# Kernel optimization log

Hardware: AMD Instinct MI355X
Metric: run time of the kernel (lower is better)

The kernel has to match this reference:

```python
import jax, jax.numpy as jnp
import numpy as np

D = 256; NH = 8; NL = 4; NP = 4; DFF = 1024
SHAPES = [(100, 100), (50, 50), (25, 25), (13, 13)]
B = 4


def layer_norm(x, g, b, eps=1e-5):
    m = x.mean(-1, keepdims=True)
    v = ((x - m) ** 2).mean(-1, keepdims=True)
    return (x - m) * jax.lax.rsqrt(v + eps) * g + b


def setup_inputs() -> dict:
    key = jax.random.key(0)
    ks = jax.random.split(key, 12)
    Lin = sum(h * w for h, w in SHAPES)  # 13294
    w = lambda k, s: jax.random.normal(k, s, jnp.float32) * 0.02
    return dict(
        src=jax.random.normal(ks[0], (B, Lin, D), jnp.float32),
        pos=0.1 * jax.random.normal(ks[1], (B, Lin, D), jnp.float32),
        reference_points=jax.random.uniform(ks[2], (B, Lin, NL, 2), dtype=jnp.float32),
        spatial_shapes=jnp.array(SHAPES, jnp.int32),
        level_start_index=jnp.array(np.cumsum([0] + [h * w for h, w in SHAPES])[:-1], jnp.int32),
        value_w=w(ks[3], (D, D)), value_b=jnp.zeros((D,), jnp.float32),
        offs_w=w(ks[4], (D, NH * NL * NP * 2)),
        offs_b=0.5 * jax.random.normal(ks[5], (NH * NL * NP * 2,), jnp.float32),
        attn_w=w(ks[6], (D, NH * NL * NP)), attn_b=jnp.zeros((NH * NL * NP,), jnp.float32),
        out_w=w(ks[7], (D, D)), out_b=jnp.zeros((D,), jnp.float32),
        ln1_g=jnp.ones((D,), jnp.float32), ln1_b=jnp.zeros((D,), jnp.float32),
        ff1_w=w(ks[8], (D, DFF)), ff1_b=jnp.zeros((DFF,), jnp.float32),
        ff2_w=w(ks[9], (DFF, D)), ff2_b=jnp.zeros((D,), jnp.float32),
        ln2_g=jnp.ones((D,), jnp.float32), ln2_b=jnp.zeros((D,), jnp.float32),
    )


def msda(query, value_in, ref, shapes, starts, value_w, value_b, offs_w, offs_b,
         attn_w, attn_b, out_w, out_b):
    Bq, Lq, Dm = query.shape
    dh = Dm // NH
    shapes_np = np.asarray(shapes); starts_np = np.asarray(starts)
    value = (value_in @ value_w + value_b).reshape(Bq, -1, NH, dh)
    offs = (query @ offs_w + offs_b).reshape(Bq, Lq, NH, NL, NP, 2)
    aw = jax.nn.softmax((query @ attn_w + attn_b).reshape(Bq, Lq, NH, NL * NP), axis=-1)
    aw = aw.reshape(Bq, Lq, NH, NL, NP)
    # offset normalizer is (W, H) per level
    normalizer = jnp.stack([shapes[:, 1], shapes[:, 0]], -1).astype(jnp.float32)
    loc = ref[:, :, None, :, None, :] + offs / normalizer[None, None, None, :, None, :]
    out = jnp.zeros((Bq, NH, Lq, dh), jnp.float32)
    for l in range(NL):
        Hl, Wl = int(shapes_np[l, 0]), int(shapes_np[l, 1])
        s = int(starts_np[l])
        v = value[:, s:s + Hl * Wl].transpose(0, 2, 1, 3)  # [B,h,HW,dh]
        x = loc[:, :, :, l, :, 0] * Wl - 0.5  # [B,Lq,h,P], align_corners=False
        y = loc[:, :, :, l, :, 1] * Hl - 0.5
        x0 = jnp.floor(x); y0 = jnp.floor(y)
        dx = x - x0; dy = y - y0
        x0i = x0.astype(jnp.int32); y0i = y0.astype(jnp.int32)
        def gather(ix, iy):
            valid = (ix >= 0) & (ix < Wl) & (iy >= 0) & (iy < Hl)  # zero padding
            idx = jnp.clip(iy, 0, Hl - 1) * Wl + jnp.clip(ix, 0, Wl - 1)
            idx = idx.transpose(0, 2, 1, 3).reshape(Bq, NH, Lq * NP)
            g = jnp.take_along_axis(v, idx[..., None], axis=2).reshape(Bq, NH, Lq, NP, dh)
            return g * valid.transpose(0, 2, 1, 3)[..., None]
        dxh = dx.transpose(0, 2, 1, 3)[..., None]
        dyh = dy.transpose(0, 2, 1, 3)[..., None]
        sampled = (gather(x0i, y0i) * (1 - dxh) * (1 - dyh)
                   + gather(x0i + 1, y0i) * dxh * (1 - dyh)
                   + gather(x0i, y0i + 1) * (1 - dxh) * dyh
                   + gather(x0i + 1, y0i + 1) * dxh * dyh)  # [B,h,Lq,P,dh]
        awl = aw[:, :, :, l].transpose(0, 2, 1, 3)[..., None]  # [B,h,Lq,P,1]
        out = out + (sampled * awl).sum(3)
    out = out.transpose(0, 2, 1, 3).reshape(Bq, Lq, Dm)
    return out @ out_w + out_b


def reference(src, pos, reference_points, spatial_shapes, level_start_index,
              value_w, value_b, offs_w, offs_b, attn_w, attn_b, out_w, out_b,
              ln1_g, ln1_b, ff1_w, ff1_b, ff2_w, ff2_b, ln2_g, ln2_b):
    # src = with_pos_embed(src, pos): NOTE this module uses (src + pos) as BOTH query and value
    q = src + pos
    src2 = msda(q, q, reference_points, spatial_shapes, level_start_index,
                value_w, value_b, offs_w, offs_b, attn_w, attn_b, out_w, out_b)
    x = layer_norm(q + src2, ln1_g, ln1_b)  # dropout is identity at eval
    ff = jnp.maximum(x @ ff1_w + ff1_b, 0.0) @ ff2_w + ff2_b
    return layer_norm(x + ff, ln2_g, ln2_b)
```

## Files before the change

### kernel.cpp

```cpp
#include <hip/hip_runtime.h>
#include <hip/hip_bf16.h>

#define B_    4
#define LIN   13294
#define M_    (B_*LIN)
#define D_    256
#define NH_   8
#define NL_   4
#define NP_   4
#define DFF_  1024

typedef __bf16 bf16;
typedef unsigned int uint;
typedef __attribute__((ext_vector_type(8))) __bf16 bfrag8;
typedef __attribute__((ext_vector_type(4))) __bf16 bf16x4;
typedef __attribute__((ext_vector_type(4))) float facc4;
typedef __attribute__((ext_vector_type(2))) float f32x2;

__global__ __launch_bounds__(256) void make_q(const float* __restrict__ src,
                                              const float* __restrict__ pos,
                                              float* __restrict__ q,
                                              bf16* __restrict__ qb, int n4) {
  int i = blockIdx.x * 256 + threadIdx.x;
  if (i >= n4) return;
  float4 s = ((const float4*)src)[i];
  float4 p = ((const float4*)pos)[i];
  float4 v = {s.x + p.x, s.y + p.y, s.z + p.z, s.w + p.w};
  ((float4*)q)[i] = v;
  bf16 t4[4] = {(bf16)v.x, (bf16)v.y, (bf16)v.z, (bf16)v.w};
  ((uint2*)qb)[i] = *(uint2*)t4;
}

__global__ __launch_bounds__(256) void prep_weights(
    const float* __restrict__ vw, const float* __restrict__ ow,
    const float* __restrict__ aw, const float* __restrict__ outw,
    const float* __restrict__ f1w, const float* __restrict__ f2w,
    const float* __restrict__ vb, const float* __restrict__ ob,
    const float* __restrict__ ab,
    bf16* __restrict__ vowt, bf16* __restrict__ outwt,
    bf16* __restrict__ f1wt, bf16* __restrict__ f2wt, float* __restrict__ vobias) {
  int seg = blockIdx.y;
  int idx = blockIdx.x * 256 + threadIdx.x;
  if (seg == 6) {
    if (idx < 256) vobias[idx] = vb[idx];
    else if (idx < 512) vobias[idx] = ob[idx - 256];
    else if (idx < 640) vobias[idx] = ab[idx - 512];
    return;
  }
  const float* W; bf16* Wt; int K, N;
  switch (seg) {
    case 0: W = vw;   Wt = vowt;              K = 256;  N = 256;  break;
    case 1: W = ow;   Wt = vowt + 256 * 256;  K = 256;  N = 256;  break;
    case 2: W = aw;   Wt = vowt + 512 * 256;  K = 256;  N = 128;  break;
    case 3: W = outw; Wt = outwt;             K = 256;  N = 256;  break;
    case 4: W = f1w;  Wt = f1wt;              K = 256;  N = 1024; break;
    default: W = f2w; Wt = f2wt;              K = 1024; N = 256;  break;
  }
  if (idx < K * N) {
    int n = idx / K, k = idx - n * K;
    Wt[idx] = (bf16)W[k * N + n];
  }
}

__device__ __forceinline__ void gload16(const bf16* g, bf16* l) {
  __builtin_amdgcn_global_load_lds(
      (const __attribute__((address_space(1))) uint*)g,
      (__attribute__((address_space(3))) uint*)l, 16, 0, 0);
}

template<int K, bool RELU>
__global__ __launch_bounds__(256) void gemm128(
    const bf16* __restrict__ A, const bf16* __restrict__ Bt,
    const float* __restrict__ bias, bf16* __restrict__ C,
    int Mdim, int N) {
  __shared__ __align__(16) bf16 As[128 * 64];
  __shared__ __align__(16) bf16 Bs[128 * 64];
  const int t = threadIdx.x, wave = t >> 6, lane = t & 63;
  const int m0 = blockIdx.x * 128, n0 = blockIdx.y * 128;
  const int wr = wave >> 1, wc = wave & 1;
  const int ln = lane & 15, quad = lane >> 4;
  const int sr = lane >> 3, cc = lane & 7;
  const int gcol = (cc ^ sr) * 8;

  const bf16* ap[4]; const bf16* bp[4];
  bf16* la[4]; bf16* lb[4];
  #pragma unroll
  for (int ii = 0; ii < 4; ii++) {
    int i = wave * 4 + ii;
    int arow = min(m0 + i * 8 + sr, Mdim - 1);
    ap[ii] = A + (size_t)arow * K + gcol;
    bp[ii] = Bt + (size_t)(n0 + i * 8 + sr) * K + gcol;
    la[ii] = As + i * 512;
    lb[ii] = Bs + i * 512;
  }
  int a_off[4], b_off[4];
  #pragma unroll
  for (int i = 0; i < 4; i++) {
    int ra = wr * 64 + i * 16 + ln;
    int rb = wc * 64 + i * 16 + ln;
    a_off[i] = ra * 128 + ((quad ^ (ra & 7)) * 16);
    b_off[i] = rb * 128 + ((quad ^ (rb & 7)) * 16);
  }

  facc4 acc[4][4];
  #pragma unroll
  for (int mt = 0; mt < 4; mt++)
    #pragma unroll
    for (int nt = 0; nt < 4; nt++) acc[mt][nt] = (facc4){0.f, 0.f, 0.f, 0.f};

  #pragma unroll 1
  for (int k0 = 0; k0 < K; k0 += 64) {
    __syncthreads();
    gload16(ap[0] + k0, la[0]); gload16(ap[1] + k0, la[1]);
    gload16(ap[2] + k0, la[2]); gload16(ap[3] + k0, la[3]);
    gload16(bp[0] + k0, lb[0]); gload16(bp[1] + k0, lb[1]);
    gload16(bp[2] + k0, lb[2]); gload16(bp[3] + k0, lb[3]);
    __syncthreads();
    #pragma unroll
    for (int ks = 0; ks < 2; ks++) {
      bfrag8 wfr[4], xfr[4];
      #pragma unroll
      for (int nt = 0; nt < 4; nt++)
        wfr[nt] = *(const bfrag8*)((const char*)Bs + (b_off[nt] ^ (ks * 64)));
      #pragma unroll
      for (int mt = 0; mt < 4; mt++)
        xfr[mt] = *(const bfrag8*)((const char*)As + (a_off[mt] ^ (ks * 64)));
      #pragma unroll
      for (int mt = 0; mt < 4; mt++)
        #pragma unroll
        for (int nt = 0; nt < 4; nt++)
          acc[mt][nt] = __builtin_amdgcn_mfma_f32_16x16x32_bf16(wfr[nt], xfr[mt], acc[mt][nt], 0, 0, 0);
    }
  }

  #pragma unroll
  for (int nt = 0; nt < 4; nt++) {
    int ncol = n0 + wc * 64 + nt * 16 + quad * 4;
    float4 bv = *(const float4*)&bias[ncol];
    #pragma unroll
    for (int mt = 0; mt < 4; mt++) {
      int row = m0 + wr * 64 + mt * 16 + ln;
      if (row < Mdim) {
        float v0 = acc[mt][nt][0] + bv.x, v1 = acc[mt][nt][1] + bv.y;
        float v2 = acc[mt][nt][2] + bv.z, v3 = acc[mt][nt][3] + bv.w;
        if (RELU) {
          v0 = fmaxf(v0, 0.f); v1 = fmaxf(v1, 0.f);
          v2 = fmaxf(v2, 0.f); v3 = fmaxf(v3, 0.f);
        }
        bf16 o[4] = {(bf16)v0, (bf16)v1, (bf16)v2, (bf16)v3};
        *(uint2*)&C[(size_t)row * N + ncol] = *(uint2*)o;
      }
    }
  }
}

__global__ __launch_bounds__(256) void msda_sample(
    const bf16* __restrict__ VOA,
    const float* __restrict__ ref,
    bf16* __restrict__ sampled) {
  int gw = (blockIdx.x * 256 + threadIdx.x) >> 6;
  int lane = threadIdx.x & 63;
  int m = gw >> 3, h = gw & 7;
  if (m >= M_) return;
  int b = m / LIN;
  int p = lane >> 2, cg = lane & 3;
  int l = p >> 2, pt = p & 3;
  int Wl = (l == 0) ? 100 : (l == 1) ? 50 : (l == 2) ? 25 : 13;
  int Hl = Wl;
  int st = (l == 0) ? 0 : (l == 1) ? 10000 : (l == 2) ? 12500 : 13125;

  const bf16* row = VOA + (size_t)m * 640;
  float e = __expf((float)row[512 + h * 16 + p]);
  float se = e;
  #pragma unroll
  for (int msk = 4; msk < 64; msk <<= 1) se += __shfl_xor(se, msk);
  float w = e / se;

  float rx = ref[((size_t)m * 4 + l) * 2 + 0];
  float ry = ref[((size_t)m * 4 + l) * 2 + 1];
  uint oxy = *(const uint*)&row[256 + ((h * 4 + l) * 4 + pt) * 2];
  float ox = __uint_as_float(oxy << 16);
  float oy = __uint_as_float(oxy & 0xffff0000u);
  float x = rx * (float)Wl + ox - 0.5f;
  float y = ry * (float)Hl + oy - 0.5f;
  float x0f = floorf(x), y0f = floorf(y);
  float dx = x - x0f, dy = y - y0f;
  int x0 = (int)x0f, y0 = (int)y0f;
  float wx1 = 1.f - dx, wy1 = 1.f - dy;

  f32x2 acc2[4];
  #pragma unroll
  for (int i = 0; i < 4; i++) acc2[i] = (f32x2){0.f, 0.f};

  size_t vbase = ((size_t)(b * LIN + st)) * 640 + h * 32 + cg * 8;
  #pragma unroll
  for (int c = 0; c < 4; c++) {
    int cx = c & 1, cy = c >> 1;
    int xi = x0 + cx, yi = y0 + cy;
    bool valid = (xi >= 0) & (xi < Wl) & (yi >= 0) & (yi < Hl);
    int xc = min(max(xi, 0), Wl - 1);
    int yc = min(max(yi, 0), Hl - 1);
    float cw = (cx ? dx : wx1) * (cy ? dy : wy1) * w;
    cw = valid ? cw : 0.f;
    uint off = (uint)(yc * Wl + xc) * 640u;
    const uint4 vv = *(const uint4*)(VOA + vbase + off);
    f32x2 cw2 = {cw, cw};
    f32x2 v0 = {__uint_as_float(vv.x << 16), __uint_as_float(vv.x & 0xffff0000u)};
    f32x2 v1 = {__uint_as_float(vv.y << 16), __uint_as_float(vv.y & 0xffff0000u)};
    f32x2 v2 = {__uint_as_float(vv.z << 16), __uint_as_float(vv.z & 0xffff0000u)};
    f32x2 v3 = {__uint_as_float(vv.w << 16), __uint_as_float(vv.w & 0xffff0000u)};
    acc2[0] = cw2 * v0 + acc2[0];
    acc2[1] = cw2 * v1 + acc2[1];
    acc2[2] = cw2 * v2 + acc2[2];
    acc2[3] = cw2 * v3 + acc2[3];
  }

  int sel = (lane >> 2) & 1;
  f32x2 sA0 = sel ? acc2[0] : acc2[2];
  f32x2 sA1 = sel ? acc2[1] : acc2[3];
  f32x2 kA0 = sel ? acc2[2] : acc2[0];
  f32x2 kA1 = sel ? acc2[3] : acc2[1];
  f32x2 rA0, rA1;
  rA0.x = __shfl_xor(sA0.x, 4); rA0.y = __shfl_xor(sA0.y, 4);
  rA1.x = __shfl_xor(sA1.x, 4); rA1.y = __shfl_xor(sA1.y, 4);
  kA0 += rA0; kA1 += rA1;

  int sel2 = (lane >> 3) & 1;
  f32x2 sB = sel2 ? kA0 : kA1;
  f32x2 kB = sel2 ? kA1 : kA0;
  f32x2 rB;
  rB.x = __shfl_xor(sB.x, 8); rB.y = __shfl_xor(sB.y, 8);
  kB += rB;

  int sel3 = (lane >> 4) & 1;
  float sC = sel3 ? kB.x : kB.y;
  float kC = sel3 ? kB.y : kB.x;
  kC += __shfl_xor(sC, 16);

  float v = kC + __shfl_xor(kC, 32);

  if (lane < 32) {
    int c = cg * 8 + ((lane >> 2) & 1) * 4 + ((lane >> 3) & 1) * 2 + ((lane >> 4) & 1);
    sampled[(size_t)m * 256 + h * 32 + c] = (bf16)v;
  }
}

__device__ inline float4 load4f(const float* p) { return *(const float4*)p; }
__device__ inline float4 load4f(const bf16* p) {
  bf16x4 v = *(const bf16x4*)p;
  float4 r = {(float)v[0], (float)v[1], (float)v[2], (float)v[3]};
  return r;
}
template<typename RT>
__global__ __launch_bounds__(256) void ln_kernel(
    const bf16* __restrict__ a, const RT* __restrict__ res,
    const float* __restrict__ g, const float* __restrict__ beta,
    float* __restrict__ out_f, bf16* __restrict__ out_b, int Mdim) {
  int wave = threadIdx.x >> 6, lane = threadIdx.x & 63;
  int row = blockIdx.x * 4 + wave;
  if (row >= Mdim) return;
  size_t base = (size_t)row * 256 + lane * 4;
  float4 av = load4f(a + base);
  float4 rv = load4f(res + base);
  float4 v = {av.x + rv.x, av.y + rv.y, av.z + rv.z, av.w + rv.w};
  float s = v.x + v.y + v.z + v.w;
  #pragma unroll
  for (int msk = 1; msk < 64; msk <<= 1) s += __shfl_xor(s, msk);
  float mean = s * (1.f / 256.f);
  float4 d = {v.x - mean, v.y - mean, v.z - mean, v.w - mean};
  float sq = d.x * d.x + d.y * d.y + d.z * d.z + d.w * d.w;
  #pragma unroll
  for (int msk = 1; msk < 64; msk <<= 1) sq += __shfl_xor(sq, msk);
  float inv = rsqrtf(sq * (1.f / 256.f) + 1e-5f);
  float4 gv = *(const float4*)(g + lane * 4);
  float4 bv = *(const float4*)(beta + lane * 4);
  float4 y = {d.x * inv * gv.x + bv.x, d.y * inv * gv.y + bv.y,
              d.z * inv * gv.z + bv.z, d.w * inv * gv.w + bv.w};
  if (out_f) *(float4*)(out_f + base) = y;
  if (out_b) {
    bf16 t4[4] = {(bf16)y.x, (bf16)y.y, (bf16)y.z, (bf16)y.w};
    *(uint2*)(out_b + base) = *(uint2*)t4;
  }
}

extern "C" void kernel_launch(void* const* d_in, const int* in_sizes, int n_in,
                              void* d_out, int out_size, void* d_ws, size_t ws_size,
                              hipStream_t stream) {
  const float* src     = (const float*)d_in[0];
  const float* pos     = (const float*)d_in[1];
  const float* refpts  = (const float*)d_in[2];
  const float* value_w = (const float*)d_in[5];
  const float* value_b = (const float*)d_in[6];
  const float* offs_w  = (const float*)d_in[7];
  const float* offs_b  = (const float*)d_in[8];
  const float* attn_w  = (const float*)d_in[9];
  const float* attn_b  = (const float*)d_in[10];
  const float* out_w   = (const float*)d_in[11];
  const float* out_b   = (const float*)d_in[12];
  const float* ln1_g   = (const float*)d_in[13];
  const float* ln1_b   = (const float*)d_in[14];
  const float* ff1_w   = (const float*)d_in[15];
  const float* ff1_b   = (const float*)d_in[16];
  const float* ff2_w   = (const float*)d_in[17];
  const float* ff2_b   = (const float*)d_in[18];
  const float* ln2_g   = (const float*)d_in[19];
  const float* ln2_b   = (const float*)d_in[20];

  char* ws = (char*)d_ws;
  size_t off = 0;
  auto take = [&](size_t bytes) -> char* {
    char* pp = ws + off;
    off += (bytes + 255) & ~(size_t)255;
    return pp;
  };
  float* q      = (float*)take((size_t)M_ * 256 * 4);
  size_t szQB   = (size_t)M_ * 256 * 2;
  size_t szVOA  = (size_t)M_ * 640 * 2;
  char* R       = take(szQB + szVOA + szQB);
  bf16* qb      = (bf16*)R;
  bf16* VOA     = (bf16*)(R + szQB);
  bf16* sampled = (bf16*)(R + szQB + szVOA);
  bf16* hb      = (bf16*)R;
  bf16* tmp     = (bf16*)take(szQB);
  bf16* x       = (bf16*)take(szQB);
  bf16* vowt    = (bf16*)take(640 * 256 * 2);
  bf16* outwt   = (bf16*)take(65536 * 2);
  bf16* f1wt    = (bf16*)take(262144 * 2);
  bf16* f2wt    = (bf16*)take(262144 * 2);
  float* vobias = (float*)take(640 * 4);
  (void)ws_size; (void)in_sizes; (void)n_in; (void)out_size;

  int n4 = M_ * 256 / 4;
  make_q<<<dim3((n4 + 255) / 256), dim3(256), 0, stream>>>(src, pos, q, qb, n4);
  prep_weights<<<dim3(1024, 7), dim3(256), 0, stream>>>(
      value_w, offs_w, attn_w, out_w, ff1_w, ff2_w, value_b, offs_b, attn_b,
      vowt, outwt, f1wt, f2wt, vobias);

  dim3 blk(256);
  int mt = (M_ + 127) / 128;
  gemm128<256, false><<<dim3(mt, 5), blk, 0, stream>>>(qb, vowt, vobias, VOA, M_, 640);
  msda_sample<<<dim3(M_ * 2), blk, 0, stream>>>(VOA, refpts, sampled);
  gemm128<256, false><<<dim3(mt, 2), blk, 0, stream>>>(sampled, outwt, out_b, tmp, M_, 256);
  ln_kernel<float><<<dim3((M_ + 3) / 4), blk, 0, stream>>>(tmp, q, ln1_g, ln1_b, nullptr, x, M_);
  gemm128<256, true><<<dim3(mt, 8), blk, 0, stream>>>(x, f1wt, ff1_b, hb, M_, 1024);
  gemm128<1024, false><<<dim3(mt, 2), blk, 0, stream>>>(hb, f2wt, ff2_b, tmp, M_, 256);
  ln_kernel<bf16><<<dim3((M_ + 3) / 4), blk, 0, stream>>>(tmp, x, ln2_g, ln2_b, (float*)d_out, nullptr, M_);
}
```

Measured before the change: 582.3 us.

## Restructure GEMMs to stage full-K A tile once and stream weights from global

Replaces the 128x128 LDS-tiled GEMM with a kernel where each block stages a 128xK(256-chunk) slice of A into padded LDS once and loops over all N columns. Weight fragments are read directly from global/L2 rather than through LDS, and grid drops the N dimension so A is read only once per row block. The change cuts redundant A traffic and per-k-step barriers, but it increases global weight loads per block, lowers parallelism (one block per 128 rows), and for K=1024 holds NB*8 accumulators in registers. The sampler also hoists its four corner loads ahead of the FMAs to expose more memory-level parallelism.

```diff
diff --git a/kernel.cpp b/kernel.cpp
--- a/kernel.cpp
+++ b/kernel.cpp
@@ -62,95 +62,115 @@
   }
 }
 
-__device__ __forceinline__ void gload16(const bf16* g, bf16* l) {
-  __builtin_amdgcn_global_load_lds(
-      (const __attribute__((address_space(1))) uint*)g,
-      (__attribute__((address_space(3))) uint*)l, 16, 0, 0);
-}
-
-template<int K, bool RELU>
-__global__ __launch_bounds__(256) void gemm128(
-    const bf16* __restrict__ A, const bf16* __restrict__ Bt,
-    const float* __restrict__ bias, bf16* __restrict__ C,
-    int Mdim, int N) {
-  __shared__ __align__(16) bf16 As[128 * 64];
-  __shared__ __align__(16) bf16 Bs[128 * 64];
+template<int K, int N, bool RELU>
+__global__ __launch_bounds__(256) void gemm_fused(
+    const bf16* __restrict__ A, const bf16* __restrict__ Wt,
+    const float* __restrict__ bias, bf16* __restrict__ C, int Mdim) {
+  static_assert(K % 256 == 0 && N % 64 == 0, "shape");
+  constexpr int NB = N / 64;
+  constexpr int PITCH = 264;
+  __shared__ __align__(16) bf16 As[128 * PITCH];
   const int t = threadIdx.x, wave = t >> 6, lane = t & 63;
-  const int m0 = blockIdx.x * 128, n0 = blockIdx.y * 128;
-  const int wr = wave >> 1, wc = wave & 1;
+  const int m0 = blockIdx.x * 128;
   const int ln = lane & 15, quad = lane >> 4;
-  const int sr = lane >> 3, cc = lane & 7;
-  const int gcol = (cc ^ sr) * 8;
-
-  const bf16* ap[4]; const bf16* bp[4];
-  bf16* la[4]; bf16* lb[4];
-  #pragma unroll
-  for (int ii = 0; ii < 4; ii++) {
-    int i = wave * 4 + ii;
-    int arow = min(m0 + i * 8 + sr, Mdim - 1);
-    ap[ii] = A + (size_t)arow * K + gcol;
-    bp[ii] = Bt + (size_t)(n0 + i * 8 + sr) * K + gcol;
-    la[ii] = As + i * 512;
-    lb[ii] = Bs + i * 512;
-  }
-  int a_off[4], b_off[4];
-  #pragma unroll
-  for (int i = 0; i < 4; i++) {
-    int ra = wr * 64 + i * 16 + ln;
-    int rb = wc * 64 + i * 16 + ln;
-    a_off[i] = ra * 128 + ((quad ^ (ra & 7)) * 16);
-    b_off[i] = rb * 128 + ((quad ^ (rb & 7)) * 16);
-  }
-
-  facc4 acc[4][4];
-  #pragma unroll
-  for (int mt = 0; mt < 4; mt++)
+
+  const char* lA0 = (const char*)As + (wave * 32 + ln) * (PITCH * 2) + quad * 16;
+  const char* lA1 = lA0 + 16 * (PITCH * 2);
+  const bf16* wbase = Wt + (size_t)ln * K + quad * 8;
+
+  auto stage = [&](int kc) {
     #pragma unroll
-    for (int nt = 0; nt < 4; nt++) acc[mt][nt] = (facc4){0.f, 0.f, 0.f, 0.f};
-
-  #pragma unroll 1
-  for (int k0 = 0; k0 < K; k0 += 64) {
-    __syncthreads();
-    gload16(ap[0] + k0, la[0]); gload16(ap[1] + k0, la[1]);
-    gload16(ap[2] + k0, la[2]); gload16(ap[3] + k0, la[3]);
-    gload16(bp[0] + k0, lb[0]); gload16(bp[1] + k0, lb[1]);
-    gload16(bp[2] + k0, lb[2]); gload16(bp[3] + k0, lb[3]);
-    __syncthreads();
+    for (int i = 0; i < 16; i++) {
+      int g = i * 256 + t;
+      int r = g >> 5, col = (g & 31) * 8;
+      uint4 v = *(const uint4*)(A + (size_t)min(m0 + r, Mdim - 1) * K + kc + col);
+      *(uint4*)(As + r * PITCH + col) = v;
+    }
+  };
+
+  auto epi = [&](int nb, facc4 (&acc)[2][4]) {
     #pragma unroll
-    for (int ks = 0; ks < 2; ks++) {
-      bfrag8 wfr[4], xfr[4];
+    for (int nt = 0; nt < 4; nt++) {
+      int ncol = nb * 64 + nt * 16 + quad * 4;
+      float4 bv = *(const float4*)&bias[ncol];
       #pragma unroll
-      for (int nt = 0; nt < 4; nt++)
-        wfr[nt] = *(const bfrag8*)((const char*)Bs + (b_off[nt] ^ (ks * 64)));
-      #pragma unroll
-      for (int mt = 0; mt < 4; mt++)
-        xfr[mt] = *(const bfrag8*)((const char*)As + (a_off[mt] ^ (ks * 64)));
-      #pragma unroll
-      for (int mt = 0; mt < 4; mt++)
-        #pragma unroll
-        for (int nt = 0; nt < 4; nt++)
-          acc[mt][nt] = __builtin_amdgcn_mfma_f32_16x16x32_bf16(wfr[nt], xfr[mt], acc[mt][nt], 0, 0, 0);
-    }
-  }
-
-  #pragma unroll
-  for (int nt = 0; nt < 4; nt++) {
-    int ncol = n0 + wc * 64 + nt * 16 + quad * 4;
-    float4 bv = *(const float4*)&bias[ncol];
-    #pragma unroll
-    for (int mt = 0; mt < 4; mt++) {
-      int row = m0 + wr * 64 + mt * 16 + ln;
-      if (row < Mdim) {
-        float v0 = acc[mt][nt][0] + bv.x, v1 = acc[mt][nt][1] + bv.y;
-        float v2 = acc[mt][nt][2] + bv.z, v3 = acc[mt][nt][3] + bv.w;
-        if (RELU) {
-          v0 = fmaxf(v0, 0.f); v1 = fmaxf(v1, 0.f);
-          v2 = fmaxf(v2, 0.f); v3 = fmaxf(v3, 0.f);
+      for (int mt = 0; mt < 2; mt++) {
+        int row = m0 + wave * 32 + mt * 16 + ln;
+        if (row < Mdim) {
+          float v0 = acc[mt][nt][0] + bv.x, v1 = acc[mt][nt][1] + bv.y;
+          float v2 = acc[mt][nt][2] + bv.z, v3 = acc[mt][nt][3] + bv.w;
+          if (RELU) {
+            v0 = fmaxf(v0, 0.f); v1 = fmaxf(v1, 0.f);
+            v2 = fmaxf(v2, 0.f); v3 = fmaxf(v3, 0.f);
+          }
+          bf16 o[4] = {(bf16)v0, (bf16)v1, (bf16)v2, (bf16)v3};
+          *(uint2*)&C[(size_t)row * N + ncol] = *(uint2*)o;
         }
-        bf16 o[4] = {(bf16)v0, (bf16)v1, (bf16)v2, (bf16)v3};
-        *(uint2*)&C[(size_t)row * N + ncol] = *(uint2*)o;
       }
     }
+  };
+
+  if constexpr (K == 256) {
+    stage(0);
+    __syncthreads();
+    #pragma unroll 1
+    for (int nb = 0; nb < NB; nb++) {
+      facc4 acc[2][4];
+      #pragma unroll
+      for (int mt = 0; mt < 2; mt++)
+        #pragma unroll
+        for (int nt = 0; nt < 4; nt++) acc[mt][nt] = (facc4){0.f, 0.f, 0.f, 0.f};
+      const bf16* wnb = wbase + (size_t)nb * 64 * K;
+      #pragma unroll
+      for (int ks = 0; ks < 8; ks++) {
+        bfrag8 wfr[4], xfr[2];
+        #pragma unroll
+        for (int nt = 0; nt < 4; nt++)
+          wfr[nt] = *(const bfrag8*)(wnb + nt * 16 * K + ks * 32);
+        xfr[0] = *(const bfrag8*)(lA0 + ks * 64);
+        xfr[1] = *(const bfrag8*)(lA1 + ks * 64);
+        #pragma unroll
+        for (int mt = 0; mt < 2; mt++)
+          #pragma unroll
+          for (int nt = 0; nt < 4; nt++)
+            acc[mt][nt] = __builtin_amdgcn_mfma_f32_16x16x32_bf16(wfr[nt], xfr[mt], acc[mt][nt], 0, 0, 0);
+      }
+      epi(nb, acc);
+    }
+  } else {
+    facc4 acc[NB][2][4];
+    #pragma unroll
+    for (int nb = 0; nb < NB; nb++)
+      #pragma unroll
+      for (int mt = 0; mt < 2; mt++)
+        #pragma unroll
+        for (int nt = 0; nt < 4; nt++) acc[nb][mt][nt] = (facc4){0.f, 0.f, 0.f, 0.f};
+    #pragma unroll 1
+    for (int kc = 0; kc < K; kc += 256) {
+      __syncthreads();
+      stage(kc);
+      __syncthreads();
+      #pragma unroll 1
+      for (int nb = 0; nb < NB; nb++) {
+        const bf16* wnb = wbase + (size_t)nb * 64 * K + kc;
+        #pragma unroll
+        for (int ks = 0; ks < 8; ks++) {
+          bfrag8 wfr[4], xfr[2];
+          #pragma unroll
+          for (int nt = 0; nt < 4; nt++)
+            wfr[nt] = *(const bfrag8*)(wnb + nt * 16 * K + ks * 32);
+          xfr[0] = *(const bfrag8*)(lA0 + ks * 64);
+          xfr[1] = *(const bfrag8*)(lA1 + ks * 64);
+          #pragma unroll
+          for (int mt = 0; mt < 2; mt++)
+            #pragma unroll
+            for (int nt = 0; nt < 4; nt++)
+              acc[nb][mt][nt] = __builtin_amdgcn_mfma_f32_16x16x32_bf16(wfr[nt], xfr[mt], acc[nb][mt][nt], 0, 0, 0);
+        }
+      }
+    }
+    #pragma unroll
+    for (int nb = 0; nb < NB; nb++) epi(nb, acc[nb]);
   }
 }
 
@@ -186,34 +206,37 @@
   float x0f = floorf(x), y0f = floorf(y);
   float dx = x - x0f, dy = y - y0f;
   int x0 = (int)x0f, y0 = (int)y0f;
-  float wx1 = 1.f - dx, wy1 = 1.f - dy;
+
+  int xc0 = min(max(x0, 0), Wl - 1), xc1 = min(max(x0 + 1, 0), Wl - 1);
+  int yc0 = min(max(y0, 0), Hl - 1), yc1 = min(max(y0 + 1, 0), Hl - 1);
+  float wx0 = ((uint)x0 < (uint)Wl) ? (1.f - dx) : 0.f;
+  float wx1 = ((uint)(x0 + 1) < (uint)Wl) ? dx : 0.f;
+  float wy0 = ((uint)y0 < (uint)Hl) ? (1.f - dy) * w : 0.f;
+  float wy1 = ((uint)(y0 + 1) < (uint)Hl) ? dy * w : 0.f;
+  float cw00 = wx0 * wy0, cw10 = wx1 * wy0, cw01 = wx0 * wy1, cw11 = wx1 * wy1;
+
+  size_t vbase = ((size_t)(b * LIN + st)) * 640 + h * 32 + cg * 8;
+  int r0 = yc0 * Wl, r1 = yc1 * Wl;
+  const uint4 v00 = *(const uint4*)(VOA + vbase + (uint)(r0 + xc0) * 640u);
+  const uint4 v10 = *(const uint4*)(VOA + vbase + (uint)(r0 + xc1) * 640u);
+  const uint4 v01 = *(const uint4*)(VOA + vbase + (uint)(r1 + xc0) * 640u);
+  const uint4 v11 = *(const uint4*)(VOA + vbase + (uint)(r1 + xc1) * 640u);
 
   f32x2 acc2[4];
   #pragma unroll
   for (int i = 0; i < 4; i++) acc2[i] = (f32x2){0.f, 0.f};
-
-  size_t vbase = ((size_t)(b * LIN + st)) * 640 + h * 32 + cg * 8;
-  #pragma unroll
-  for (int c = 0; c < 4; c++) {
-    int cx = c & 1, cy = c >> 1;
-    int xi = x0 + cx, yi = y0 + cy;
-    bool valid = (xi >= 0) & (xi < Wl) & (yi >= 0) & (yi < Hl);
-    int xc = min(max(xi, 0), Wl - 1);
-    int yc = min(max(yi, 0), Hl - 1);
-    float cw = (cx ? dx : wx1) * (cy ? dy : wy1) * w;
-    cw = valid ? cw : 0.f;
-    uint off = (uint)(yc * Wl + xc) * 640u;
-    const uint4 vv = *(const uint4*)(VOA + vbase + off);
+  auto fmac = [&](const uint4& vv, float cw) {
     f32x2 cw2 = {cw, cw};
-    f32x2 v0 = {__uint_as_float(vv.x << 16), __uint_as_float(vv.x & 0xffff0000u)};
-    f32x2 v1 = {__uint_as_float(vv.y << 16), __uint_as_float(vv.y & 0xffff0000u)};
-    f32x2 v2 = {__uint_as_float(vv.z << 16), __uint_as_float(vv.z & 0xffff0000u)};
-    f32x2 v3 = {__uint_as_float(vv.w << 16), __uint_as_float(vv.w & 0xffff0000u)};
-    acc2[0] = cw2 * v0 + acc2[0];
-    acc2[1] = cw2 * v1 + acc2[1];
-    acc2[2] = cw2 * v2 + acc2[2];
-    acc2[3] = cw2 * v3 + acc2[3];
-  }
+    f32x2 u0 = {__uint_as_float(vv.x << 16), __uint_as_float(vv.x & 0xffff0000u)};
+    f32x2 u1 = {__uint_as_float(vv.y << 16), __uint_as_float(vv.y & 0xffff0000u)};
+    f32x2 u2 = {__uint_as_float(vv.z << 16), __uint_as_float(vv.z & 0xffff0000u)};
+    f32x2 u3 = {__uint_as_float(vv.w << 16), __uint_as_float(vv.w & 0xffff0000u)};
+    acc2[0] = cw2 * u0 + acc2[0];
+    acc2[1] = cw2 * u1 + acc2[1];
+    acc2[2] = cw2 * u2 + acc2[2];
+    acc2[3] = cw2 * u3 + acc2[3];
+  };
+  fmac(v00, cw00); fmac(v10, cw10); fmac(v01, cw01); fmac(v11, cw11);
 
   int sel = (lane >> 2) & 1;
   f32x2 sA0 = sel ? acc2[0] : acc2[2];
@@ -338,11 +361,11 @@
 
   dim3 blk(256);
   int mt = (M_ + 127) / 128;
-  gemm128<256, false><<<dim3(mt, 5), blk, 0, stream>>>(qb, vowt, vobias, VOA, M_, 640);
+  gemm_fused<256, 640, false><<<dim3(mt), blk, 0, stream>>>(qb, vowt, vobias, VOA, M_);
   msda_sample<<<dim3(M_ * 2), blk, 0, stream>>>(VOA, refpts, sampled);
-  gemm128<256, false><<<dim3(mt, 2), blk, 0, stream>>>(sampled, outwt, out_b, tmp, M_, 256);
+  gemm_fused<256, 256, false><<<dim3(mt), blk, 0, stream>>>(sampled, outwt, out_b, tmp, M_);
   ln_kernel<float><<<dim3((M_ + 3) / 4), blk, 0, stream>>>(tmp, q, ln1_g, ln1_b, nullptr, x, M_);
-  gemm128<256, true><<<dim3(mt, 8), blk, 0, stream>>>(x, f1wt, ff1_b, hb, M_, 1024);
-  gemm128<1024, false><<<dim3(mt, 2), blk, 0, stream>>>(hb, f2wt, ff2_b, tmp, M_, 256);
+  gemm_fused<256, 1024, true><<<dim3(mt), blk, 0, stream>>>(x, f1wt, ff1_b, hb, M_);
+  gemm_fused<1024, 256, false><<<dim3(mt), blk, 0, stream>>>(hb, f2wt, ff2_b, tmp, M_);
   ln_kernel<bf16><<<dim3((M_ + 3) / 4), blk, 0, stream>>>(tmp, x, ln2_g, ln2_b, (float*)d_out, nullptr, M_);
 }
```

After: 1.020 ms. +75.1%, slower.
